# Optimization experiments

Hardware: AMD Instinct MI355X
Metric: run time of the kernel (lower is better)

## Reference

```python
import math
import jax, jax.numpy as jnp
import numpy as np

B, T, S = 4, 4096, 1024
HID, CTX, EMB, H = 1024, 768, 1024, 16
D = EMB // H  # head_dim = 64


def setup_inputs() -> dict:
    key = jax.random.key(0)
    ks = jax.random.split(key, 7)
    sc = lambda n: 1.0 / math.sqrt(n)
    return {
        "tokens": jax.random.normal(ks[0], (B, T, HID), jnp.float32),
        "context": jax.random.normal(ks[1], (B, S, CTX), jnp.float32),
        "Wq": jax.random.normal(ks[2], (HID, EMB), jnp.float32) * sc(HID),
        "Wk": jax.random.normal(ks[3], (CTX, EMB), jnp.float32) * sc(CTX),
        "Wv": jax.random.normal(ks[4], (CTX, EMB), jnp.float32) * sc(CTX),
        "Wo": jax.random.normal(ks[5], (EMB, HID), jnp.float32) * sc(EMB),
        "bo": jnp.zeros((HID,), jnp.float32),
    }


def reference(tokens, context, Wq, Wk, Wv, Wo, bo):
    # projections (bias-free, as in torch Linear(bias=False))
    Q = tokens @ Wq              # [B,T,EMB]
    K = context @ Wk             # [B,S,EMB]
    V = context @ Wv             # [B,S,EMB]
    # split heads: B T (H D) -> B H T D
    Q = Q.reshape(B, T, H, D).transpose(0, 2, 1, 3)
    K = K.reshape(B, S, H, D).transpose(0, 2, 1, 3)
    V = V.reshape(B, S, H, D).transpose(0, 2, 1, 3)
    scores = jnp.einsum('bhtd,bhsd->bhts', Q, K) / math.sqrt(D)
    attn = jax.nn.softmax(scores, axis=-1)
    ctx = jnp.einsum('bhts,bhsd->bhtd', attn, V)
    ctx = ctx.transpose(0, 2, 1, 3).reshape(B, T, EMB)
    return ctx @ Wo + bo
```

## Files before the change

### kernel.cpp

```cpp
#include <hip/hip_runtime.h>
#include <hip/hip_bf16.h>

#define B_ 4
#define T_ 4096
#define S_ 1024
#define HID_ 1024
#define CTX_ 768
#define EMB_ 1024
#define H_ 16
#define D_ 64

#define QSCALE 0.18033688011112042f

typedef __attribute__((ext_vector_type(8))) short short8;
typedef __attribute__((ext_vector_type(4))) float f32x4;
typedef __attribute__((ext_vector_type(4))) unsigned short us4;
typedef unsigned short ushort_t;

__device__ inline ushort_t f2b(float f) {
  union { float f; unsigned u; } x; x.f = f;
  return (ushort_t)((x.u + 0x7fffu + ((x.u >> 16) & 1u)) >> 16);
}
__device__ inline unsigned cvtpk2(float a, float b) {
  __hip_bfloat162 h = __float22bfloat162_rn(float2{a, b});
  union { __hip_bfloat162 h; unsigned u; } c; c.h = h; return c.u;
}
__device__ inline ushort_t f2b_fast(float f) {
  __hip_bfloat16 h = __float2bfloat16(f);
  union { __hip_bfloat16 h; ushort_t u; } c; c.h = h; return c.u;
}

using gu32p = const __attribute__((address_space(1))) unsigned int*;
using lu32p = __attribute__((address_space(3))) unsigned int*;
__device__ inline void gload16(const ushort_t* g, ushort_t* l) {
  __builtin_amdgcn_global_load_lds((gu32p)(const void*)g, (lu32p)(void*)l, 16, 0, 0);
}

__device__ inline void conv_body(const float* __restrict__ in, ushort_t* __restrict__ out,
                                 int blk, int tid) {
  const size_t i = ((size_t)blk * 256 + tid) * 8;
  const float4 a = *(const float4*)(in + i);
  const float4 b = *(const float4*)(in + i + 4);
  uint4 u;
  u.x = cvtpk2(a.x, a.y); u.y = cvtpk2(a.z, a.w);
  u.z = cvtpk2(b.x, b.y); u.w = cvtpk2(b.z, b.w);
  *(uint4*)(out + i) = u;
}

__device__ inline void convT_body(const float* __restrict__ W, ushort_t* __restrict__ Wt,
                                  int K, int tile, int tid, float (*Ls)[33]) {
  const int n0 = (tile & 31) * 32, k0 = (tile >> 5) * 32;
  const int r = tid >> 3, c4 = (tid & 7) * 4;
  const float4 v = *(const float4*)&W[(size_t)(k0 + r) * 1024 + n0 + c4];
  Ls[r][c4] = v.x; Ls[r][c4 + 1] = v.y; Ls[r][c4 + 2] = v.z; Ls[r][c4 + 3] = v.w;
  __syncthreads();
  us4 o;
  o.x = f2b_fast(Ls[c4][r]);     o.y = f2b_fast(Ls[c4 + 1][r]);
  o.z = f2b_fast(Ls[c4 + 2][r]); o.w = f2b_fast(Ls[c4 + 3][r]);
  *(us4*)&Wt[(size_t)(n0 + r) * K + k0 + c4] = o;
}

__global__ __launch_bounds__(256) void prepA(
    const float* __restrict__ tokens, const float* __restrict__ context,
    const float* __restrict__ Wq, const float* __restrict__ Wk,
    const float* __restrict__ Wv,
    ushort_t* __restrict__ Tok, ushort_t* __restrict__ CtxB,
    ushort_t* __restrict__ WqT, ushort_t* __restrict__ WkvT)
{
  __shared__ float Ls[32][33];
  const int tid = threadIdx.x;
  int blk = (int)blockIdx.x;
  if (blk < 8192) { conv_body(tokens, Tok, blk, tid); return; }
  blk -= 8192;
  if (blk < 1536) { conv_body(context, CtxB, blk, tid); return; }
  blk -= 1536;
  if (blk < 1024) { convT_body(Wq, WqT, 1024, blk, tid, Ls); return; }
  blk -= 1024;
  if (blk < 768)  { convT_body(Wk, WkvT, 768, blk, tid, Ls); return; }
  blk -= 768;
  convT_body(Wv, WkvT + (size_t)1024 * 768, 768, blk, tid, Ls);
}

__global__ __launch_bounds__(256) void prepO(const float* __restrict__ Wo,
                                             ushort_t* __restrict__ WoT) {
  __shared__ float Ls[32][33];
  convT_body(Wo, WoT, 1024, (int)blockIdx.x, threadIdx.x, Ls);
}

__global__ __launch_bounds__(256) void gemm128kv(
    const ushort_t* __restrict__ A, const ushort_t* __restrict__ Bt,
    ushort_t* __restrict__ Kb, ushort_t* __restrict__ Vtb)
{
  __shared__ ushort_t As[128 * 32];
  __shared__ ushort_t Bs[128 * 32];
  const int Kd = CTX_;
  const int tid = threadIdx.x;
  const int bn = blockIdx.x, bm = blockIdx.y;
  const int lane = tid & 63, w = tid >> 6;
  const int lr = lane & 15, lg = lane >> 4;
  const int wr = w >> 1, wc = w & 1;

  f32x4 acc[4][4] = {};

  const int srow = tid >> 2, scol = (tid & 3) * 8;
  const ushort_t* ga = A + (size_t)(bm * 128 + srow) * Kd + scol;
  const ushort_t* gb = Bt + (size_t)(bn * 128 + srow) * Kd + scol;
  ushort_t* la = &As[tid * 8];
  ushort_t* lb = &Bs[tid * 8];
  const size_t rstep = (size_t)64 * Kd;

  for (int k0 = 0; k0 < Kd; k0 += 32) {
    gload16(ga + k0, la);
    gload16(ga + k0 + rstep, la + 2048);
    gload16(gb + k0, lb);
    gload16(gb + k0 + rstep, lb + 2048);
    __syncthreads();
    short8 af[4], bf[4];
#pragma unroll
    for (int m = 0; m < 4; ++m)
      af[m] = *(const short8*)&As[(wr * 64 + m * 16 + lr) * 32 + lg * 8];
#pragma unroll
    for (int n = 0; n < 4; ++n)
      bf[n] = *(const short8*)&Bs[(wc * 64 + n * 16 + lr) * 32 + lg * 8];
#pragma unroll
    for (int m = 0; m < 4; ++m)
#pragma unroll
      for (int n = 0; n < 4; ++n)
        acc[m][n] = __builtin_amdgcn_mfma_f32_16x16x32_bf16(af[m], bf[n], acc[m][n], 0, 0, 0);
    __syncthreads();
  }

  const int row0 = bm * 128 + wr * 64 + lg * 4;
  const int col0 = bn * 128 + wc * 64 + lr;

  if (col0 < 1024) {
#pragma unroll
    for (int m = 0; m < 4; ++m)
#pragma unroll
      for (int n = 0; n < 4; ++n) {
        const int col = col0 + n * 16;
#pragma unroll
        for (int i = 0; i < 4; ++i)
          Kb[(size_t)(row0 + m * 16 + i) * EMB_ + col] = f2b_fast(acc[m][n][i]);
      }
  } else {
#pragma unroll
    for (int m = 0; m < 4; ++m) {
      const int rbase = row0 + m * 16;
      const int bb = rbase >> 10;
      const int s0 = rbase & (S_ - 1);
#pragma unroll
      for (int n = 0; n < 4; ++n) {
        const int vc = col0 + n * 16 - 1024;
        const int hh = vc >> 6, dd = vc & 63;
        us4 o;
        o.x = f2b_fast(acc[m][n][0]); o.y = f2b_fast(acc[m][n][1]);
        o.z = f2b_fast(acc[m][n][2]); o.w = f2b_fast(acc[m][n][3]);
        *(us4*)&Vtb[(((size_t)bb * H_ + hh) * D_ + dd) * S_ + s0] = o;
      }
    }
  }
}

template<int EPI>
__global__ __launch_bounds__(512) void gemm256(
    const ushort_t* __restrict__ A, const ushort_t* __restrict__ Bt,
    void* __restrict__ Cp, const float* __restrict__ bias,
    int M, int Kd, int N)
{
  extern __shared__ ushort_t L[];
  const int tid = threadIdx.x;
  const int lane = tid & 63, wid = tid >> 6;
  const int lr = lane & 15, lg = lane >> 4;
  const int wm = wid >> 2, wn = wid & 3;

  const int cpx = (int)gridDim.x >> 3;
  const int lin = (int)blockIdx.x;
  const int swz = (lin & 7) * cpx + (lin >> 3);
  const int nbn = N >> 8;
  const int bm = swz / nbn, bn = swz % nbn;

  const int sr = tid >> 2;
  const int csrc = (tid & 3) ^ ((sr >> 1) & 3);
  const ushort_t* gA = A + (size_t)(bm * 256 + sr) * Kd + csrc * 8;
  const ushort_t* gB = Bt + (size_t)(bn * 256 + sr) * Kd + csrc * 8;
  const size_t half = (size_t)128 * Kd;
  ushort_t* const dA = L + tid * 8;
  ushort_t* const dB = L + 8192 + tid * 8;

  f32x4 acc[8][4] = {};
  const int NT = Kd >> 5;

#define STAGE256(c) do {                                \
    const int slot_ = ((c) & 3) * 16384;                \
    const int k0_ = (c) << 5;                           \
    gload16(gA + k0_, dA + slot_);                      \
    gload16(gA + k0_ + half, dA + slot_ + 4096);        \
    gload16(gB + k0_, dB + slot_);                      \
    gload16(gB + k0_ + half, dB + slot_ + 4096);        \
  } while (0)

  STAGE256(0); STAGE256(1); STAGE256(2);
  asm volatile("s_waitcnt vmcnt(8)" ::: "memory");
  __builtin_amdgcn_s_barrier();
  __builtin_amdgcn_sched_barrier(0);

  for (int t = 0; t < NT; ++t) {
    if (t + 3 < NT) STAGE256(t + 3);
    const ushort_t* As_ = L + (t & 3) * 16384;
    const ushort_t* Bs_ = As_ + 8192;
    short8 af[8], bf[4];
#pragma unroll
    for (int m = 0; m < 8; ++m) {
      const int row = wm * 128 + m * 16 + lr;
      af[m] = *(const short8*)&As_[row * 32 + (lg ^ ((row >> 1) & 3)) * 8];
    }
#pragma unroll
    for (int n = 0; n < 4; ++n) {
      const int row = wn * 64 + n * 16 + lr;
      bf[n] = *(const short8*)&Bs_[row * 32 + (lg ^ ((row >> 1) & 3)) * 8];
    }
    __builtin_amdgcn_s_setprio(1);
#pragma unroll
    for (int m = 0; m < 8; ++m)
#pragma unroll
      for (int n = 0; n < 4; ++n)
        acc[m][n] = __builtin_amdgcn_mfma_f32_16x16x32_bf16(af[m], bf[n], acc[m][n], 0, 0, 0);
    __builtin_amdgcn_s_setprio(0);
    asm volatile("s_waitcnt vmcnt(8)" ::: "memory");
    __builtin_amdgcn_s_barrier();
    __builtin_amdgcn_sched_barrier(0);
  }
#undef STAGE256

  const int row0 = bm * 256 + wm * 128 + lg * 4;
  const int col0 = bn * 256 + wn * 64 + lr;

  if constexpr (EPI == 3) {
    float* C = (float*)Cp;
#pragma unroll
    for (int n = 0; n < 4; ++n) {
      const int col = col0 + n * 16;
      const float bv = bias[col];
#pragma unroll
      for (int m = 0; m < 8; ++m)
#pragma unroll
        for (int i = 0; i < 4; ++i)
          C[(size_t)(row0 + m * 16 + i) * N + col] = acc[m][n][i] + bv;
    }
  } else {
    ushort_t* C = (ushort_t*)Cp;
#pragma unroll
    for (int m = 0; m < 8; ++m)
#pragma unroll
      for (int n = 0; n < 4; ++n) {
        const int col = col0 + n * 16;
#pragma unroll
        for (int i = 0; i < 4; ++i)
          C[(size_t)(row0 + m * 16 + i) * N + col] = f2b(acc[m][n][i] * QSCALE);
      }
  }
}

__global__ __launch_bounds__(512) void attn_v5r(
    const ushort_t* __restrict__ Q, const ushort_t* __restrict__ K,
    const ushort_t* __restrict__ Vt, ushort_t* __restrict__ C)
{
  __shared__ ushort_t Ks[2][64 * 64];
  __shared__ ushort_t Vs[2][64 * 64];
  __shared__ ushort_t Ps[8][16][72];
  const int tid = threadIdx.x;
  const int lane = tid & 63, w = tid >> 6;
  const int lr = lane & 15, lg = lane >> 4;

  const int bid = (int)blockIdx.x;
  const int g = (bid & 7) | (((bid >> 3) >> 4) << 3);
  const int tb = (bid >> 3) & 15;
  const int h = g & 15, b = g >> 4;
  const int t0 = tb * 256;

  short8 qf[2][2];
#pragma unroll
  for (int qs = 0; qs < 2; ++qs) {
    const size_t qrow = (size_t)b * T_ + t0 + w * 32 + qs * 16 + lr;
    const ushort_t* qp = Q + qrow * EMB_ + h * 64;
    qf[qs][0] = *(const short8*)(qp + lg * 8);
    qf[qs][1] = *(const short8*)(qp + 32 + lg * 8);
  }

  short8 ones;
#pragma unroll
  for (int j = 0; j < 8; ++j) ones[j] = (short)0x3F80;

  f32x4 o[2][4] = {};
  f32x4 lacc[2] = {};

  const int srow = tid >> 3, schunk = tid & 7;
  const int sswz = schunk ^ (srow & 7);
  const ushort_t* kg = K + ((size_t)b * S_ + srow) * EMB_ + h * 64 + sswz * 8;
  const ushort_t* vg = Vt + (((size_t)b * H_ + h) * D_ + srow) * S_ + sswz * 8;

  gload16(kg, &Ks[0][tid * 8]);
  gload16(vg, &Vs[0][tid * 8]);

  int cur = 0;
  for (int st = 0; st < S_ / 64; ++st) {
    __syncthreads();
    if (st + 1 < S_ / 64) {
      gload16(kg + (size_t)(st + 1) * 64 * EMB_, &Ks[cur ^ 1][tid * 8]);
      gload16(vg + (st + 1) * 64, &Vs[cur ^ 1][tid * 8]);
    }

    f32x4 sacc[2][4] = {};
    __builtin_amdgcn_s_setprio(1);
#pragma unroll
    for (int c = 0; c < 4; ++c) {
      const int krow = c * 16 + lr;
      const int sw = krow & 7;
      const short8 ka0 = *(const short8*)&Ks[cur][krow * 64 + ((lg ^ sw) * 8)];
      const short8 ka1 = *(const short8*)&Ks[cur][krow * 64 + (((4 + lg) ^ sw) * 8)];
#pragma unroll
      for (int qs = 0; qs < 2; ++qs) {
        sacc[qs][c] = __builtin_amdgcn_mfma_f32_16x16x32_bf16(ka0, qf[qs][0], sacc[qs][c], 0, 0, 0);
        sacc[qs][c] = __builtin_amdgcn_mfma_f32_16x16x32_bf16(ka1, qf[qs][1], sacc[qs][c], 0, 0, 0);
      }
    }
    __builtin_amdgcn_s_setprio(0);

    short8 pa[2][2];
#pragma unroll
    for (int qs = 0; qs < 2; ++qs) {
#pragma unroll
      for (int c = 0; c < 4; ++c) {
        uint2 pk;
        pk.x = cvtpk2(exp2f(sacc[qs][c][0]), exp2f(sacc[qs][c][1]));
        pk.y = cvtpk2(exp2f(sacc[qs][c][2]), exp2f(sacc[qs][c][3]));
        *(uint2*)&Ps[w][lr][c * 16 + lg * 4] = pk;
      }
      pa[qs][0] = *(const short8*)&Ps[w][lr][lg * 8];
      pa[qs][1] = *(const short8*)&Ps[w][lr][32 + lg * 8];
    }

    __builtin_amdgcn_s_setprio(1);
#pragma unroll
    for (int sh = 0; sh < 2; ++sh) {
#pragma unroll
      for (int dc = 0; dc < 4; ++dc) {
        const int vrow = dc * 16 + lr;
        const int vsw = vrow & 7;
        const short8 vb = *(const short8*)&Vs[cur][vrow * 64 + (((sh * 4 + lg) ^ vsw) * 8)];
        o[0][dc] = __builtin_amdgcn_mfma_f32_16x16x32_bf16(pa[0][sh], vb, o[0][dc], 0, 0, 0);
        o[1][dc] = __builtin_amdgcn_mfma_f32_16x16x32_bf16(pa[1][sh], vb, o[1][dc], 0, 0, 0);
      }
      lacc[0] = __builtin_amdgcn_mfma_f32_16x16x32_bf16(pa[0][sh], ones, lacc[0], 0, 0, 0);
      lacc[1] = __builtin_amdgcn_mfma_f32_16x16x32_bf16(pa[1][sh], ones, lacc[1], 0, 0, 0);
    }
    __builtin_amdgcn_s_setprio(0);

    cur ^= 1;
  }

#pragma unroll
  for (int qs = 0; qs < 2; ++qs) {
#pragma unroll
    for (int i = 0; i < 4; ++i) {
      const float li = 1.0f / lacc[qs][i];
      const size_t trow = (size_t)b * T_ + t0 + w * 32 + qs * 16 + lg * 4 + i;
#pragma unroll
      for (int dc = 0; dc < 4; ++dc)
        C[trow * EMB_ + h * 64 + dc * 16 + lr] = f2b_fast(o[qs][dc][i] * li);
    }
  }
}

extern "C" void kernel_launch(void* const* d_in, const int* in_sizes, int n_in,
                              void* d_out, int out_size, void* d_ws, size_t ws_size,
                              hipStream_t stream) {
  const float* tokens  = (const float*)d_in[0];
  const float* context = (const float*)d_in[1];
  const float* Wq = (const float*)d_in[2];
  const float* Wk = (const float*)d_in[3];
  const float* Wv = (const float*)d_in[4];
  const float* Wo = (const float*)d_in[5];
  const float* bo = (const float*)d_in[6];
  float* out = (float*)d_out;

  ushort_t* Qb  = (ushort_t*)d_out;
  ushort_t* Tok = Qb + (size_t)B_ * T_ * EMB_;
  ushort_t* Kb   = (ushort_t*)d_ws;
  ushort_t* Vtb  = Kb + (size_t)B_ * S_ * EMB_;
  ushort_t* Cb   = Vtb + (size_t)B_ * S_ * EMB_;
  ushort_t* WqT  = Cb + (size_t)B_ * T_ * EMB_;
  ushort_t* WkvT = WqT + (size_t)EMB_ * HID_;

  prepA<<<12288, 256, 0, stream>>>(tokens, context, Wq, Wk, Wv,
                                   Tok, Cb, WqT, WkvT);
  gemm256<1><<<dim3((B_ * T_ / 256) * (EMB_ / 256)), 512, 131072, stream>>>(
      Tok, WqT, Qb, nullptr, B_ * T_, HID_, EMB_);
  prepO<<<1024, 256, 0, stream>>>(Wo, WqT);
  gemm128kv<<<dim3(16, 32), 256, 0, stream>>>(Cb, WkvT, Kb, Vtb);
  attn_v5r<<<dim3((T_ / 256) * H_ * B_), 512, 0, stream>>>(Qb, Kb, Vtb, Cb);
  gemm256<3><<<dim3((B_ * T_ / 256) * (HID_ / 256)), 512, 131072, stream>>>(
      Cb, WqT, out, bo, B_ * T_, EMB_, HID_);
}
```

Baseline: 229.5 us.

## Switch attention to 32x32x16 MFMA with cross-lane P repack instead of LDS

Rewrites the attention inner loop to use 32x32x16 bf16 MFMA tiles (one 32-row tile per wave) instead of 16x16x32 tiles. The P matrix is now converted from the S accumulator layout to the A-operand layout with permlane32_swap (or shuffles as a fallback) rather than a round trip through per-wave LDS. This removes the Ps scratch buffer and its LDS traffic, and cuts the number of MFMA issues. It also adds launch bounds targeting higher occupancy. The costs are larger accumulator register usage and a different output write pattern.

```diff
diff --git a/kernel.cpp b/kernel.cpp
--- a/kernel.cpp
+++ b/kernel.cpp
@@ -14,7 +14,9 @@
 
 typedef __attribute__((ext_vector_type(8))) short short8;
 typedef __attribute__((ext_vector_type(4))) float f32x4;
+typedef __attribute__((ext_vector_type(16))) float f32x16;
 typedef __attribute__((ext_vector_type(4))) unsigned short us4;
+typedef __attribute__((ext_vector_type(2))) int i32x2;
 typedef unsigned short ushort_t;
 
 __device__ inline ushort_t f2b(float f) {
@@ -262,16 +264,15 @@
   }
 }
 
-__global__ __launch_bounds__(512) void attn_v5r(
+__global__ __launch_bounds__(512, 4) void attn_v7(
     const ushort_t* __restrict__ Q, const ushort_t* __restrict__ K,
     const ushort_t* __restrict__ Vt, ushort_t* __restrict__ C)
 {
-  __shared__ ushort_t Ks[2][64 * 64];
-  __shared__ ushort_t Vs[2][64 * 64];
-  __shared__ ushort_t Ps[8][16][72];
+  __shared__ ushort_t Ks[2][4096];
+  __shared__ ushort_t Vs[2][4096];
   const int tid = threadIdx.x;
   const int lane = tid & 63, w = tid >> 6;
-  const int lr = lane & 15, lg = lane >> 4;
+  const int t_ = lane & 31, hi = lane >> 5;
 
   const int bid = (int)blockIdx.x;
   const int g = (bid & 7) | (((bid >> 3) >> 4) << 3);
@@ -279,21 +280,27 @@
   const int h = g & 15, b = g >> 4;
   const int t0 = tb * 256;
 
-  short8 qf[2][2];
-#pragma unroll
-  for (int qs = 0; qs < 2; ++qs) {
-    const size_t qrow = (size_t)b * T_ + t0 + w * 32 + qs * 16 + lr;
-    const ushort_t* qp = Q + qrow * EMB_ + h * 64;
-    qf[qs][0] = *(const short8*)(qp + lg * 8);
-    qf[qs][1] = *(const short8*)(qp + 32 + lg * 8);
+  short8 qf[4];
+  {
+    const size_t qrow = (size_t)b * T_ + t0 + w * 32 + t_;
+    const ushort_t* qp = Q + qrow * EMB_ + h * 64 + hi * 8;
+#pragma unroll
+    for (int kd = 0; kd < 4; ++kd)
+      qf[kd] = *(const short8*)(qp + kd * 16);
   }
 
   short8 ones;
 #pragma unroll
   for (int j = 0; j < 8; ++j) ones[j] = (short)0x3F80;
 
-  f32x4 o[2][4] = {};
-  f32x4 lacc[2] = {};
+  f32x16 o0 = {}, o1 = {}, lacc = {};
+
+  int roff[2][4];
+#pragma unroll
+  for (int x = 0; x < 2; ++x)
+#pragma unroll
+    for (int y = 0; y < 4; ++y)
+      roff[x][y] = (x * 32 + t_) * 64 + (((2 * y + hi) ^ (t_ & 7)) * 8);
 
   const int srow = tid >> 3, schunk = tid & 7;
   const int sswz = schunk ^ (srow & 7);
@@ -311,49 +318,52 @@
       gload16(vg + (st + 1) * 64, &Vs[cur ^ 1][tid * 8]);
     }
 
-    f32x4 sacc[2][4] = {};
+    f32x16 sacc0 = {}, sacc1 = {};
     __builtin_amdgcn_s_setprio(1);
 #pragma unroll
-    for (int c = 0; c < 4; ++c) {
-      const int krow = c * 16 + lr;
-      const int sw = krow & 7;
-      const short8 ka0 = *(const short8*)&Ks[cur][krow * 64 + ((lg ^ sw) * 8)];
-      const short8 ka1 = *(const short8*)&Ks[cur][krow * 64 + (((4 + lg) ^ sw) * 8)];
-#pragma unroll
-      for (int qs = 0; qs < 2; ++qs) {
-        sacc[qs][c] = __builtin_amdgcn_mfma_f32_16x16x32_bf16(ka0, qf[qs][0], sacc[qs][c], 0, 0, 0);
-        sacc[qs][c] = __builtin_amdgcn_mfma_f32_16x16x32_bf16(ka1, qf[qs][1], sacc[qs][c], 0, 0, 0);
-      }
+    for (int kd = 0; kd < 4; ++kd) {
+      const short8 ka0 = *(const short8*)&Ks[cur][roff[0][kd]];
+      const short8 ka1 = *(const short8*)&Ks[cur][roff[1][kd]];
+      sacc0 = __builtin_amdgcn_mfma_f32_32x32x16_bf16(ka0, qf[kd], sacc0, 0, 0, 0);
+      sacc1 = __builtin_amdgcn_mfma_f32_32x32x16_bf16(ka1, qf[kd], sacc1, 0, 0, 0);
     }
     __builtin_amdgcn_s_setprio(0);
 
-    short8 pa[2][2];
-#pragma unroll
-    for (int qs = 0; qs < 2; ++qs) {
-#pragma unroll
-      for (int c = 0; c < 4; ++c) {
-        uint2 pk;
-        pk.x = cvtpk2(exp2f(sacc[qs][c][0]), exp2f(sacc[qs][c][1]));
-        pk.y = cvtpk2(exp2f(sacc[qs][c][2]), exp2f(sacc[qs][c][3]));
-        *(uint2*)&Ps[w][lr][c * 16 + lg * 4] = pk;
-      }
-      pa[qs][0] = *(const short8*)&Ps[w][lr][lg * 8];
-      pa[qs][1] = *(const short8*)&Ps[w][lr][32 + lg * 8];
+    short8 pa[4];
+#pragma unroll
+    for (int ks = 0; ks < 4; ++ks) {
+      const f32x16 sv = (ks < 2) ? sacc0 : sacc1;
+      const int q = (ks & 1) * 8;
+      float E[8];
+#pragma unroll
+      for (int r = 0; r < 8; ++r) E[r] = exp2f(sv[q + r]);
+      const unsigned A0 = cvtpk2(E[0], E[1]), A1 = cvtpk2(E[2], E[3]);
+      const unsigned B0 = cvtpk2(E[4], E[5]), B1 = cvtpk2(E[6], E[7]);
+      union { unsigned u[4]; short8 s; } pp;
+#if __has_builtin(__builtin_amdgcn_permlane32_swap)
+      const i32x2 r02 = __builtin_amdgcn_permlane32_swap((int)A0, (int)B0, false, false);
+      const i32x2 r13 = __builtin_amdgcn_permlane32_swap((int)A1, (int)B1, false, false);
+      pp.u[0] = (unsigned)r02[0]; pp.u[1] = (unsigned)r13[0];
+      pp.u[2] = (unsigned)r02[1]; pp.u[3] = (unsigned)r13[1];
+#else
+      const unsigned sA0 = (unsigned)__shfl_xor((int)A0, 32);
+      const unsigned sB0 = (unsigned)__shfl_xor((int)B0, 32);
+      const unsigned sA1 = (unsigned)__shfl_xor((int)A1, 32);
+      const unsigned sB1 = (unsigned)__shfl_xor((int)B1, 32);
+      pp.u[0] = hi ? sB0 : A0;  pp.u[1] = hi ? sB1 : A1;
+      pp.u[2] = hi ? B0 : sA0;  pp.u[3] = hi ? B1 : sA1;
+#endif
+      pa[ks] = pp.s;
     }
 
     __builtin_amdgcn_s_setprio(1);
 #pragma unroll
-    for (int sh = 0; sh < 2; ++sh) {
-#pragma unroll
-      for (int dc = 0; dc < 4; ++dc) {
-        const int vrow = dc * 16 + lr;
-        const int vsw = vrow & 7;
-        const short8 vb = *(const short8*)&Vs[cur][vrow * 64 + (((sh * 4 + lg) ^ vsw) * 8)];
-        o[0][dc] = __builtin_amdgcn_mfma_f32_16x16x32_bf16(pa[0][sh], vb, o[0][dc], 0, 0, 0);
-        o[1][dc] = __builtin_amdgcn_mfma_f32_16x16x32_bf16(pa[1][sh], vb, o[1][dc], 0, 0, 0);
-      }
-      lacc[0] = __builtin_amdgcn_mfma_f32_16x16x32_bf16(pa[0][sh], ones, lacc[0], 0, 0, 0);
-      lacc[1] = __builtin_amdgcn_mfma_f32_16x16x32_bf16(pa[1][sh], ones, lacc[1], 0, 0, 0);
+    for (int ks = 0; ks < 4; ++ks) {
+      const short8 vb0 = *(const short8*)&Vs[cur][roff[0][ks]];
+      const short8 vb1 = *(const short8*)&Vs[cur][roff[1][ks]];
+      o0 = __builtin_amdgcn_mfma_f32_32x32x16_bf16(pa[ks], vb0, o0, 0, 0, 0);
+      o1 = __builtin_amdgcn_mfma_f32_32x32x16_bf16(pa[ks], vb1, o1, 0, 0, 0);
+      lacc = __builtin_amdgcn_mfma_f32_32x32x16_bf16(pa[ks], ones, lacc, 0, 0, 0);
     }
     __builtin_amdgcn_s_setprio(0);
 
@@ -361,15 +371,13 @@
   }
 
 #pragma unroll
-  for (int qs = 0; qs < 2; ++qs) {
-#pragma unroll
-    for (int i = 0; i < 4; ++i) {
-      const float li = 1.0f / lacc[qs][i];
-      const size_t trow = (size_t)b * T_ + t0 + w * 32 + qs * 16 + lg * 4 + i;
-#pragma unroll
-      for (int dc = 0; dc < 4; ++dc)
-        C[trow * EMB_ + h * 64 + dc * 16 + lr] = f2b_fast(o[qs][dc][i] * li);
-    }
+  for (int reg = 0; reg < 16; ++reg) {
+    const float li = 1.0f / lacc[reg];
+    const int r = (reg & 3) + 8 * (reg >> 2) + 4 * hi;
+    const size_t trow = (size_t)b * T_ + t0 + w * 32 + r;
+    ushort_t* cp = C + trow * EMB_ + h * 64 + t_;
+    cp[0]  = f2b_fast(o0[reg] * li);
+    cp[32] = f2b_fast(o1[reg] * li);
   }
 }
 
@@ -399,7 +407,7 @@
       Tok, WqT, Qb, nullptr, B_ * T_, HID_, EMB_);
   prepO<<<1024, 256, 0, stream>>>(Wo, WqT);
   gemm128kv<<<dim3(16, 32), 256, 0, stream>>>(Cb, WkvT, Kb, Vtb);
-  attn_v5r<<<dim3((T_ / 256) * H_ * B_), 512, 0, stream>>>(Qb, Kb, Vtb, Cb);
+  attn_v7<<<dim3((T_ / 256) * H_ * B_), 512, 0, stream>>>(Qb, Kb, Vtb, Cb);
   gemm256<3><<<dim3((B_ * T_ / 256) * (HID_ / 256)), 512, 131072, stream>>>(
       Cb, WqT, out, bo, B_ * T_, EMB_, HID_);
 }
```

Measured after the change: 235.9 us. +2.8%, slower.

## Fuse fp32-to-bf16 token conversion into the Q projection GEMM loads

Applied to the files above, without the earlier changes.

Removes the separate pass that converted the fp32 tokens tensor to bf16. A new GEMM variant loads fp32 A tiles straight into registers, converts them to bf16 and writes them to shared memory, while B tiles keep using the direct global-to-LDS loads. This saves a full write and re-read of a 32 MB-class intermediate, at the cost of twice the A-side global load bytes inside the GEMM and a register-staged software pipeline that may raise register pressure.

```diff
diff --git a/kernel.cpp b/kernel.cpp
--- a/kernel.cpp
+++ b/kernel.cpp
@@ -61,17 +61,15 @@
 }
 
 __global__ __launch_bounds__(256) void prepA(
-    const float* __restrict__ tokens, const float* __restrict__ context,
+    const float* __restrict__ context,
     const float* __restrict__ Wq, const float* __restrict__ Wk,
     const float* __restrict__ Wv,
-    ushort_t* __restrict__ Tok, ushort_t* __restrict__ CtxB,
-    ushort_t* __restrict__ WqT, ushort_t* __restrict__ WkvT)
+    ushort_t* __restrict__ CtxB, ushort_t* __restrict__ WqT,
+    ushort_t* __restrict__ WkvT)
 {
   __shared__ float Ls[32][33];
   const int tid = threadIdx.x;
   int blk = (int)blockIdx.x;
-  if (blk < 8192) { conv_body(tokens, Tok, blk, tid); return; }
-  blk -= 8192;
   if (blk < 1536) { conv_body(context, CtxB, blk, tid); return; }
   blk -= 1536;
   if (blk < 1024) { convT_body(Wq, WqT, 1024, blk, tid, Ls); return; }
@@ -262,6 +260,124 @@
   }
 }
 
+__global__ __launch_bounds__(512) void gemm256f(
+    const float* __restrict__ Af, const ushort_t* __restrict__ Bt,
+    ushort_t* __restrict__ Cp, int M, int N)
+{
+  constexpr int Kd = 1024, NT = 32;
+  extern __shared__ ushort_t L[];
+  const int tid = threadIdx.x;
+  const int lane = tid & 63, wid = tid >> 6;
+  const int lr = lane & 15, lg = lane >> 4;
+  const int wm = wid >> 2, wn = wid & 3;
+
+  const int cpx = (int)gridDim.x >> 3;
+  const int lin = (int)blockIdx.x;
+  const int swz = (lin & 7) * cpx + (lin >> 3);
+  const int nbn = N >> 8;
+  const int bm = swz / nbn, bn = swz % nbn;
+
+  const int sr = tid >> 2;
+  const int csrc = (tid & 3) ^ ((sr >> 1) & 3);
+  const float* gA = Af + (size_t)(bm * 256 + sr) * Kd + csrc * 8;
+  const ushort_t* gB = Bt + (size_t)(bn * 256 + sr) * Kd + csrc * 8;
+  const size_t half = (size_t)128 * Kd;
+  ushort_t* const dA = L + tid * 8;
+  ushort_t* const dB = L + 8192 + tid * 8;
+
+  f32x4 acc[8][4] = {};
+  float4 ra0[4], ra1[4];
+
+#define ALOADF(c, RS) do { const int k0_ = (c) << 5;      \
+    RS[0] = *(const float4*)(gA + k0_);                   \
+    RS[1] = *(const float4*)(gA + k0_ + 4);               \
+    RS[2] = *(const float4*)(gA + k0_ + half);            \
+    RS[3] = *(const float4*)(gA + k0_ + half + 4);        \
+  } while (0)
+
+#define AWRITE(c, RS) do { const int slot_ = ((c) & 3) * 16384;  \
+    uint4 u0, u1;                                                \
+    u0.x = cvtpk2(RS[0].x, RS[0].y); u0.y = cvtpk2(RS[0].z, RS[0].w); \
+    u0.z = cvtpk2(RS[1].x, RS[1].y); u0.w = cvtpk2(RS[1].z, RS[1].w); \
+    u1.x = cvtpk2(RS[2].x, RS[2].y); u1.y = cvtpk2(RS[2].z, RS[2].w); \
+    u1.z = cvtpk2(RS[3].x, RS[3].y); u1.w = cvtpk2(RS[3].z, RS[3].w); \
+    *(uint4*)(dA + slot_) = u0;                                  \
+    *(uint4*)(dA + slot_ + 4096) = u1;                           \
+  } while (0)
+
+#define BSTAGE(c) do { const int slot_ = ((c) & 3) * 16384; const int k0_ = (c) << 5; \
+    gload16(gB + k0_, dB + slot_);                      \
+    gload16(gB + k0_ + half, dB + slot_ + 4096);        \
+  } while (0)
+
+#define COMPUTE(c) do {                                                  \
+    const ushort_t* As_ = L + ((c) & 3) * 16384;                         \
+    const ushort_t* Bs_ = As_ + 8192;                                    \
+    short8 af[8], bf[4];                                                 \
+    _Pragma("unroll")                                                    \
+    for (int m = 0; m < 8; ++m) {                                        \
+      const int row = wm * 128 + m * 16 + lr;                            \
+      af[m] = *(const short8*)&As_[row * 32 + (lg ^ ((row >> 1) & 3)) * 8]; \
+    }                                                                    \
+    _Pragma("unroll")                                                    \
+    for (int n = 0; n < 4; ++n) {                                        \
+      const int row = wn * 64 + n * 16 + lr;                             \
+      bf[n] = *(const short8*)&Bs_[row * 32 + (lg ^ ((row >> 1) & 3)) * 8]; \
+    }                                                                    \
+    __builtin_amdgcn_s_setprio(1);                                       \
+    _Pragma("unroll")                                                    \
+    for (int m = 0; m < 8; ++m)                                          \
+      _Pragma("unroll")                                                  \
+      for (int n = 0; n < 4; ++n)                                        \
+        acc[m][n] = __builtin_amdgcn_mfma_f32_16x16x32_bf16(af[m], bf[n], acc[m][n], 0, 0, 0); \
+    __builtin_amdgcn_s_setprio(0);                                       \
+  } while (0)
+
+#define ENDBAR do {                                        \
+    asm volatile("s_waitcnt lgkmcnt(0)" ::: "memory");     \
+    __builtin_amdgcn_s_barrier();                          \
+    __builtin_amdgcn_sched_barrier(0);                     \
+  } while (0)
+
+  {
+    float4 p0[4], p1[4], p2[4];
+    ALOADF(0, p0); ALOADF(1, p1); ALOADF(2, p2);
+    AWRITE(0, p0); AWRITE(1, p1); AWRITE(2, p2);
+    BSTAGE(0); BSTAGE(1); BSTAGE(2);
+    ALOADF(3, ra1);
+    asm volatile("s_waitcnt vmcnt(4)" ::: "memory");
+    ENDBAR;
+  }
+
+  for (int t = 0; t < NT; t += 2) {
+    if (t + 3 < NT) { AWRITE(t + 3, ra1); BSTAGE(t + 3); }
+    if (t + 4 < NT) ALOADF(t + 4, ra0);
+    COMPUTE(t);
+    ENDBAR;
+    if (t + 4 < NT) { AWRITE(t + 4, ra0); BSTAGE(t + 4); }
+    if (t + 5 < NT) ALOADF(t + 5, ra1);
+    COMPUTE(t + 1);
+    ENDBAR;
+  }
+#undef ALOADF
+#undef AWRITE
+#undef BSTAGE
+#undef COMPUTE
+#undef ENDBAR
+
+  const int row0 = bm * 256 + wm * 128 + lg * 4;
+  const int col0 = bn * 256 + wn * 64 + lr;
+#pragma unroll
+  for (int m = 0; m < 8; ++m)
+#pragma unroll
+    for (int n = 0; n < 4; ++n) {
+      const int col = col0 + n * 16;
+#pragma unroll
+      for (int i = 0; i < 4; ++i)
+        Cp[(size_t)(row0 + m * 16 + i) * N + col] = f2b(acc[m][n][i] * QSCALE);
+    }
+}
+
 __global__ __launch_bounds__(512) void attn_v5r(
     const ushort_t* __restrict__ Q, const ushort_t* __restrict__ K,
     const ushort_t* __restrict__ Vt, ushort_t* __restrict__ C)
@@ -386,17 +502,15 @@
   float* out = (float*)d_out;
 
   ushort_t* Qb  = (ushort_t*)d_out;
-  ushort_t* Tok = Qb + (size_t)B_ * T_ * EMB_;
   ushort_t* Kb   = (ushort_t*)d_ws;
   ushort_t* Vtb  = Kb + (size_t)B_ * S_ * EMB_;
   ushort_t* Cb   = Vtb + (size_t)B_ * S_ * EMB_;
   ushort_t* WqT  = Cb + (size_t)B_ * T_ * EMB_;
   ushort_t* WkvT = WqT + (size_t)EMB_ * HID_;
 
-  prepA<<<12288, 256, 0, stream>>>(tokens, context, Wq, Wk, Wv,
-                                   Tok, Cb, WqT, WkvT);
-  gemm256<1><<<dim3((B_ * T_ / 256) * (EMB_ / 256)), 512, 131072, stream>>>(
-      Tok, WqT, Qb, nullptr, B_ * T_, HID_, EMB_);
+  prepA<<<4096, 256, 0, stream>>>(context, Wq, Wk, Wv, Cb, WqT, WkvT);
+  gemm256f<<<dim3((B_ * T_ / 256) * (EMB_ / 256)), 512, 131072, stream>>>(
+      tokens, WqT, Qb, B_ * T_, EMB_);
   prepO<<<1024, 256, 0, stream>>>(Wo, WqT);
   gemm128kv<<<dim3(16, 32), 256, 0, stream>>>(Cb, WkvT, Kb, Vtb);
   attn_v5r<<<dim3((T_ / 256) * H_ * B_), 512, 0, stream>>>(Qb, Kb, Vtb, Cb);
```

New measurement: 231.2 us. Within noise of the previous version (+0.8%).
